# Kernel tuning notes

Hardware: AMD Instinct MI355X
Metric: run time of the kernel (lower is better)

The kernel has to match this reference:

```python
import jax, jax.numpy as jnp
import numpy as np

N = 100000   # nodes
E = 600000   # edges
B = 512      # graphs in batch
H = 128      # hidden dim
ED = 8       # edge feature dim
TWO48 = float(2 ** 48 - 1)


def _w(k, shape, fan_in):
    return jax.random.normal(k, shape, jnp.float32) * (1.0 / np.sqrt(fan_in))


def setup_inputs() -> dict:
    key = jax.random.key(0)
    ks = jax.random.split(key, 32)
    inp = {}
    inp["s_node_ids"] = jax.random.randint(ks[0], (N,), 0, 2 ** 31 - 1, dtype=jnp.int32)
    inp["s_edge_index"] = jax.random.randint(ks[1], (2, E), 0, N, dtype=jnp.int32)
    inp["s_edge_attr"] = jax.random.normal(ks[2], (E, ED), jnp.float32)
    inp["s_batch"] = jnp.sort(jax.random.randint(ks[3], (N,), 0, B, dtype=jnp.int32))
    inp["depth"] = jax.random.uniform(ks[4], (B,), jnp.float32)
    # id_mlp: Linear(1,H) -> ReLU -> Linear(H,H)
    inp["id_w1"] = _w(ks[5], (1, H), 1); inp["id_b1"] = jnp.zeros((H,), jnp.float32)
    inp["id_w2"] = _w(ks[6], (H, H), H); inp["id_b2"] = jnp.zeros((H,), jnp.float32)
    # edge_mlp: Linear(ED,H) -> ReLU -> Linear(H,H)
    inp["ed_w1"] = _w(ks[7], (ED, H), ED); inp["ed_b1"] = jnp.zeros((H,), jnp.float32)
    inp["ed_w2"] = _w(ks[8], (H, H), H); inp["ed_b2"] = jnp.zeros((H,), jnp.float32)
    # GINEConv nn MLPs: Linear(H,H) -> ReLU -> Linear(H,H)
    inp["c1_w1"] = _w(ks[9], (H, H), H); inp["c1_b1"] = jnp.zeros((H,), jnp.float32)
    inp["c1_w2"] = _w(ks[10], (H, H), H); inp["c1_b2"] = jnp.zeros((H,), jnp.float32)
    inp["c2_w1"] = _w(ks[11], (H, H), H); inp["c2_b1"] = jnp.zeros((H,), jnp.float32)
    inp["c2_w2"] = _w(ks[12], (H, H), H); inp["c2_b2"] = jnp.zeros((H,), jnp.float32)
    inp["rg_w1"] = _w(ks[13], (H + 1, H), H + 1); inp["rg_b1"] = jnp.zeros((H,), jnp.float32)
    inp["rg_w2"] = _w(ks[14], (H, 1), H); inp["rg_b2"] = jnp.zeros((1,), jnp.float32)
    return inp


def _mlp2(x, w1, b1, w2, b2):
    return jax.nn.relu(x @ w1 + b1) @ w2 + b2


def _gine(x, src, dst, e, w1, b1, w2, b2):
    # message = ReLU(x_j + e), sum-aggregated at dst; out = nn((1+eps)*x + aggr), eps=0
    msg = jax.nn.relu(x[src] + e)                       # [E, H]
    aggr = jax.ops.segment_sum(msg, dst, num_segments=N)  # [N, H]
    return _mlp2(x + aggr, w1, b1, w2, b2)


def _global_mean(x, batch):
    sums = jax.ops.segment_sum(x, batch, num_segments=B)                          # [B, H]
    cnts = jax.ops.segment_sum(jnp.ones((x.shape[0], 1), x.dtype), batch, num_segments=B)
    return sums / jnp.maximum(cnts, 1.0)


def reference(s_node_ids, s_edge_index, s_edge_attr, s_batch, depth,
              id_w1, id_b1, id_w2, id_b2,
              ed_w1, ed_b1, ed_w2, ed_b2,
              c1_w1, c1_b1, c1_w2, c1_b2,
              c2_w1, c2_b1, c2_w2, c2_b2,
              rg_w1, rg_b1, rg_w2, rg_b2):
    src, dst = s_edge_index[0], s_edge_index[1]
    x0 = jnp.clip(s_node_ids.astype(jnp.float32) / TWO48, 0.0, 1.0)[:, None]  # [N,1]
    x = _mlp2(x0, id_w1, id_b1, id_w2, id_b2)                                 # [N,H]
    e = _mlp2(s_edge_attr, ed_w1, ed_b1, ed_w2, ed_b2)                        # [E,H]
    x = jax.nn.relu(_gine(x, src, dst, e, c1_w1, c1_b1, c1_w2, c1_b2))
    x = jax.nn.relu(_gine(x, src, dst, e, c2_w1, c2_b1, c2_w2, c2_b2))
    rep = jnp.concatenate([_global_mean(x, s_batch), depth[:, None]], axis=1)  # [B,H+1]
    return _mlp2(rep, rg_w1, rg_b1, rg_w2, rg_b2)[:, 0]                        # [B]
```

## Files before the change

kernel.cpp:

```cpp
#include <hip/hip_runtime.h>
#include <hip/hip_bf16.h>

#define N_NODES 100000
#define N_EDGES 600000
#define NB      512
#define H       128
#define ED      8
#define SCAN_CHUNK 1024
#define N_CHUNKS   98

typedef __attribute__((ext_vector_type(8))) short short8;
typedef __attribute__((ext_vector_type(4))) float f32x4;
typedef __attribute__((ext_vector_type(4))) unsigned int u32x4;
typedef unsigned short u16;
typedef unsigned int   u32;

static __device__ __forceinline__ u16 f2bf(float f) {
    u32 u = __float_as_uint(f);
    u32 r = u + 0x7fffu + ((u >> 16) & 1u);
    return (u16)(r >> 16);
}
static __device__ __forceinline__ float bf2f(u32 h) {
    return __uint_as_float(h << 16);
}
static __device__ __forceinline__ u32 bfpack(float lo, float hi) {
    u32 r;
    asm("v_cvt_pk_bf16_f32 %0, %1, %2" : "=v"(r) : "v"(lo), "v"(hi));
    return r;
}

__global__ __launch_bounds__(256) void pack_hist_kernel(
    const float* __restrict__ W0, const float* __restrict__ W1,
    const float* __restrict__ W2, const float* __restrict__ W3,
    const float* __restrict__ W4, const float* __restrict__ W5,
    const float* __restrict__ W6,
    short8* __restrict__ O0, short8* __restrict__ O1,
    short8* __restrict__ O2, short8* __restrict__ O3,
    short8* __restrict__ O4, short8* __restrict__ O5,
    short8* __restrict__ O6,
    const int* __restrict__ edge_index, int* __restrict__ counts)
{
    if (blockIdx.x >= 50) {
        int e = (blockIdx.x - 50) * 256 + threadIdx.x;
        if (e < N_EDGES) atomicAdd(&counts[edge_index[N_EDGES + e]], 1);
        return;
    }
    int gid = blockIdx.x * 256 + threadIdx.x;
    const float* W; short8* O; int Krows, kkmax, slot;
    if (gid < 512) { W = W0; O = O0; Krows = ED; kkmax = 1; slot = gid; }
    else {
        int m = (gid - 512) / 2048;
        slot = (gid - 512) % 2048;
        Krows = H; kkmax = 4;
        switch (m) {
            case 0: W = W1; O = O1; break;
            case 1: W = W2; O = O2; break;
            case 2: W = W3; O = O3; break;
            case 3: W = W4; O = O4; break;
            case 4: W = W5; O = O5; break;
            default: W = W6; O = O6; break;
        }
    }
    int lane = slot & 63;
    int t = slot >> 6;
    int nt = t & 1; t >>= 1;
    int kk = t % kkmax;
    int w  = t / kkmax;
    int quad = lane >> 4, n15 = lane & 15;
    int n = w * 32 + nt * 16 + n15;
    short8 v;
    #pragma unroll
    for (int j = 0; j < 8; j++) {
        int k = kk * 32 + quad * 8 + j;
        v[j] = (k < Krows) ? (short)f2bf(W[k * H + n]) : (short)0;
    }
    O[slot] = v;
}

__global__ __launch_bounds__(256) void scan_node_kernel(
    const int* __restrict__ counts, int* __restrict__ chunk_scan,
    int* __restrict__ bsum_raw,
    const int* __restrict__ ids,
    const float* __restrict__ w1, const float* __restrict__ b1,
    const short8* __restrict__ pW2, const float* __restrict__ b2,
    u16* __restrict__ x_out)
{
    __shared__ u16 sH[64 * 136];
    __shared__ float s_x0[64];
    __shared__ int sS[256];
    int tid = threadIdx.x;

    if (blockIdx.x < N_CHUNKS) {
        int base = blockIdx.x * SCAN_CHUNK + tid * 4;
        int4 v = *(const int4*)&counts[base];
        int q0 = v.x, q1 = q0 + v.y, q2 = q1 + v.z, q3 = q2 + v.w;
        sS[tid] = q3;
        __syncthreads();
        #pragma unroll
        for (int off = 1; off < 256; off <<= 1) {
            int t = (tid >= off) ? sS[tid - off] : 0;
            __syncthreads();
            sS[tid] += t;
            __syncthreads();
        }
        int excl = sS[tid] - q3;
        int4 o;
        o.x = excl; o.y = excl + q0; o.z = excl + q1; o.w = excl + q2;
        *(int4*)&chunk_scan[base] = o;
        if (tid == 255) bsum_raw[blockIdx.x] = sS[255];
        return;
    }

    int bid = blockIdx.x - N_CHUNKS;
    int w = tid >> 6, lane = tid & 63, quad = lane >> 4, n15 = lane & 15;
    short8 fW2[4][2];
    #pragma unroll
    for (int kk = 0; kk < 4; kk++) {
        fW2[kk][0] = pW2[((w * 4 + kk) * 2 + 0) * 64 + lane];
        fW2[kk][1] = pW2[((w * 4 + kk) * 2 + 1) * 64 + lane];
    }
    float rb2[2] = { b2[w * 32 + n15], b2[w * 32 + 16 + n15] };
    float w1c = w1[tid & 127], b1c = b1[tid & 127];
    const int ntile = (N_NODES + 63) / 64;
    for (int tile = bid; tile < ntile; tile += 768) {
        int row0 = tile * 64;
        if (tid < 64) {
            int n = row0 + tid;
            float x0 = (n < N_NODES) ? (float)ids[n] / 281474976710655.0f : 0.0f;
            s_x0[tid] = fminf(fmaxf(x0, 0.0f), 1.0f);
        }
        __syncthreads();
        int half = tid >> 7, c = tid & 127;
        #pragma unroll
        for (int rr = 0; rr < 32; rr += 2) {
            int r = half + rr * 2;
            u32 p = bfpack(fmaxf(s_x0[r] * w1c + b1c, 0.0f),
                           fmaxf(s_x0[r + 2] * w1c + b1c, 0.0f));
            sH[r * 136 + c]       = (u16)p;
            sH[(r + 2) * 136 + c] = (u16)(p >> 16);
        }
        __syncthreads();
        f32x4 acc[4][2];
        #pragma unroll
        for (int s = 0; s < 4; s++) { acc[s][0] = (f32x4){0,0,0,0}; acc[s][1] = (f32x4){0,0,0,0}; }
        #pragma unroll
        for (int kk = 0; kk < 4; kk++) {
            #pragma unroll
            for (int s = 0; s < 4; s++) {
                short8 a = *(const short8*)&sH[(s * 16 + n15) * 136 + kk * 32 + quad * 8];
                acc[s][0] = __builtin_amdgcn_mfma_f32_16x16x32_bf16(a, fW2[kk][0], acc[s][0], 0, 0, 0);
                acc[s][1] = __builtin_amdgcn_mfma_f32_16x16x32_bf16(a, fW2[kk][1], acc[s][1], 0, 0, 0);
            }
        }
        __syncthreads();
        #pragma unroll
        for (int s = 0; s < 4; s++)
            #pragma unroll
            for (int nt = 0; nt < 2; nt++) {
                int col = w * 32 + nt * 16 + n15;
                int rb = (s * 16 + quad * 4) * 136 + col;
                u32 p0 = bfpack(acc[s][nt][0] + rb2[nt], acc[s][nt][1] + rb2[nt]);
                u32 p1 = bfpack(acc[s][nt][2] + rb2[nt], acc[s][nt][3] + rb2[nt]);
                sH[rb]       = (u16)p0;
                sH[rb + 136] = (u16)(p0 >> 16);
                sH[rb + 272] = (u16)p1;
                sH[rb + 408] = (u16)(p1 >> 16);
            }
        __syncthreads();
        for (int idx = tid; idx < 64 * 16; idx += 256) {
            int r = idx >> 4, c8 = (idx & 15) << 3;
            int n = row0 + r;
            if (n < N_NODES)
                *(uint4*)&x_out[(long)n * H + c8] = *(const uint4*)&sH[r * 136 + c8];
        }
        __syncthreads();
    }
}

__global__ __launch_bounds__(256) void fill_kernel(
    const int* __restrict__ edge_index,
    const int* __restrict__ chunk_scan, const int* __restrict__ bsum_raw,
    int* __restrict__ counts, int* __restrict__ src_list,
    const float* __restrict__ attr, u16* __restrict__ attr_perm)
{
    __shared__ int sB[128];
    int tid = threadIdx.x;
    int v0 = 0;
    if (tid < 128) {
        v0 = (tid < N_CHUNKS) ? bsum_raw[tid] : 0;
        sB[tid] = v0;
    }
    __syncthreads();
    #pragma unroll
    for (int off = 1; off < 128; off <<= 1) {
        int t = (tid < 128 && tid >= off) ? sB[tid - off] : 0;
        __syncthreads();
        if (tid < 128) sB[tid] += t;
        __syncthreads();
    }
    if (tid < 128) sB[tid] -= v0;
    __syncthreads();

    int e = blockIdx.x * 256 + tid;
    if (e >= N_EDGES) return;
    int src = edge_index[e];
    int dst = edge_index[N_EDGES + e];
    int slot = atomicAdd(&counts[dst], -1) - 1;
    int pos = chunk_scan[dst] + sB[dst >> 10] + slot;
    src_list[pos] = src;
    float4 a0 = *(const float4*)&attr[(long)e * ED];
    float4 a1 = *(const float4*)&attr[(long)e * ED + 4];
    u32 w0 = bfpack(a0.x, a0.y);
    u32 w1 = bfpack(a0.z, a0.w);
    u32 w2 = bfpack(a1.x, a1.y);
    u32 w3 = bfpack(a1.z, a1.w);
    *(uint4*)&attr_perm[(long)pos * ED] = make_uint4(w0, w1, w2, w3);
}

__global__ __launch_bounds__(256) void edge_mlp_mfma(
    const u16* __restrict__ attr_perm,
    const int* __restrict__ chunk_scan, const int* __restrict__ bsum_raw,
    int* __restrict__ row_start,
    const short8* __restrict__ pW1, const float* __restrict__ b1,
    const short8* __restrict__ pW2, const float* __restrict__ b2,
    u16* __restrict__ e_perm)
{
    __shared__ u16 sH[64 * 136];
    __shared__ int sB[128];
    int tid = threadIdx.x;

    if (blockIdx.x < 392) {
        int v0 = 0;
        if (tid < 128) {
            v0 = (tid < N_CHUNKS) ? bsum_raw[tid] : 0;
            sB[tid] = v0;
        }
        __syncthreads();
        #pragma unroll
        for (int off = 1; off < 128; off <<= 1) {
            int t = (tid < 128 && tid >= off) ? sB[tid - off] : 0;
            __syncthreads();
            if (tid < 128) sB[tid] += t;
            __syncthreads();
        }
        if (tid < 128) sB[tid] -= v0;
        __syncthreads();
        int i = blockIdx.x * 256 + tid;
        if (i <= N_NODES) row_start[i] = chunk_scan[i] + sB[i >> 10];
        __syncthreads();
    }

    int w = tid >> 6, lane = tid & 63, quad = lane >> 4, n15 = lane & 15;
    short8 fW1[2];
    fW1[0] = pW1[(w * 2 + 0) * 64 + lane];
    fW1[1] = pW1[(w * 2 + 1) * 64 + lane];
    short8 fW2[4][2];
    #pragma unroll
    for (int kk = 0; kk < 4; kk++) {
        fW2[kk][0] = pW2[((w * 4 + kk) * 2 + 0) * 64 + lane];
        fW2[kk][1] = pW2[((w * 4 + kk) * 2 + 1) * 64 + lane];
    }
    float rb1[2] = { b1[w * 32 + n15], b1[w * 32 + 16 + n15] };
    float rb2[2] = { b2[w * 32 + n15], b2[w * 32 + 16 + n15] };
    const short8 zero8 = (short8){0,0,0,0,0,0,0,0};
    const int ntile = N_EDGES / 64;
    for (int tile = blockIdx.x; tile < ntile; tile += gridDim.x) {
        int row0 = tile * 64;
        short8 av[4];
        #pragma unroll
        for (int s = 0; s < 4; s++) {
            av[s] = zero8;
            if (quad == 0)
                av[s] = *(const short8*)&attr_perm[(long)(row0 + s * 16 + n15) * ED];
        }
        f32x4 acc[4][2];
        #pragma unroll
        for (int s = 0; s < 4; s++) { acc[s][0] = (f32x4){0,0,0,0}; acc[s][1] = (f32x4){0,0,0,0}; }
        #pragma unroll
        for (int s = 0; s < 4; s++) {
            acc[s][0] = __builtin_amdgcn_mfma_f32_16x16x32_bf16(av[s], fW1[0], acc[s][0], 0, 0, 0);
            acc[s][1] = __builtin_amdgcn_mfma_f32_16x16x32_bf16(av[s], fW1[1], acc[s][1], 0, 0, 0);
        }
        #pragma unroll
        for (int s = 0; s < 4; s++)
            #pragma unroll
            for (int nt = 0; nt < 2; nt++) {
                int col = w * 32 + nt * 16 + n15;
                int rb = (s * 16 + quad * 4) * 136 + col;
                u32 p0 = bfpack(fmaxf(acc[s][nt][0] + rb1[nt], 0.0f),
                                fmaxf(acc[s][nt][1] + rb1[nt], 0.0f));
                u32 p1 = bfpack(fmaxf(acc[s][nt][2] + rb1[nt], 0.0f),
                                fmaxf(acc[s][nt][3] + rb1[nt], 0.0f));
                sH[rb]       = (u16)p0;
                sH[rb + 136] = (u16)(p0 >> 16);
                sH[rb + 272] = (u16)p1;
                sH[rb + 408] = (u16)(p1 >> 16);
            }
        __syncthreads();
        #pragma unroll
        for (int s = 0; s < 4; s++) { acc[s][0] = (f32x4){0,0,0,0}; acc[s][1] = (f32x4){0,0,0,0}; }
        #pragma unroll
        for (int kk = 0; kk < 4; kk++) {
            #pragma unroll
            for (int s = 0; s < 4; s++) {
                short8 a = *(const short8*)&sH[(s * 16 + n15) * 136 + kk * 32 + quad * 8];
                acc[s][0] = __builtin_amdgcn_mfma_f32_16x16x32_bf16(a, fW2[kk][0], acc[s][0], 0, 0, 0);
                acc[s][1] = __builtin_amdgcn_mfma_f32_16x16x32_bf16(a, fW2[kk][1], acc[s][1], 0, 0, 0);
            }
        }
        __syncthreads();
        #pragma unroll
        for (int s = 0; s < 4; s++)
            #pragma unroll
            for (int nt = 0; nt < 2; nt++) {
                int col = w * 32 + nt * 16 + n15;
                int rb = (s * 16 + quad * 4) * 136 + col;
                u32 p0 = bfpack(acc[s][nt][0] + rb2[nt], acc[s][nt][1] + rb2[nt]);
                u32 p1 = bfpack(acc[s][nt][2] + rb2[nt], acc[s][nt][3] + rb2[nt]);
                sH[rb]       = (u16)p0;
                sH[rb + 136] = (u16)(p0 >> 16);
                sH[rb + 272] = (u16)p1;
                sH[rb + 408] = (u16)(p1 >> 16);
            }
        __syncthreads();
        for (int idx = tid; idx < 64 * 16; idx += 256) {
            int r = idx >> 4, c8 = (idx & 15) << 3;
            *(uint4*)&e_perm[(long)(row0 + r) * H + c8] = *(const uint4*)&sH[r * 136 + c8];
        }
        __syncthreads();
    }
}

static __device__ __forceinline__ void acc8(float* a, u32x4 xv, u32x4 ev) {
    #pragma unroll
    for (int q = 0; q < 4; q++) {
        a[2 * q + 0] += fmaxf(bf2f(xv[q] & 0xffff) + bf2f(ev[q] & 0xffff), 0.0f);
        a[2 * q + 1] += fmaxf(bf2f(xv[q] >> 16)    + bf2f(ev[q] >> 16),    0.0f);
    }
}

__global__ __launch_bounds__(256) void aggregate_kernel(
    const int* __restrict__ row_start,
    const int* __restrict__ src_list,
    const u16* __restrict__ e_perm,
    const u16* __restrict__ x,
    u16* __restrict__ xs_out)
{
    int tid  = threadIdx.x;
    int lane = tid & 63;
    int l16  = lane & 15;
    int base = lane & 48;
    int fo   = l16 * 8;
    int n = blockIdx.x * 16 + (tid >> 4);
    const u16* xb = x + fo;

    int beg = row_start[n];
    int end = row_start[n + 1];
    float a[8], b[8];
    #pragma unroll
    for (int q = 0; q < 8; q++) { a[q] = 0.0f; b[q] = 0.0f; }

    for (int j0 = beg; j0 < end; j0 += 16) {
        int m = min(16, end - j0);
        int sv = src_list[j0 + min(l16, m - 1)];
        const u16* ej = e_perm + (long)j0 * H + fo;
        int j = 0;
        for (; j + 2 <= m; j += 2) {
            int s0 = __shfl(sv, base | j);
            int s1 = __shfl(sv, base | (j + 1));
            u32x4 xv0 = *(const u32x4*)(xb + (long)s0 * H);
            u32x4 ev0 = *(const u32x4*)(ej + (long)(j + 0) * H);
            u32x4 xv1 = *(const u32x4*)(xb + (long)s1 * H);
            u32x4 ev1 = *(const u32x4*)(ej + (long)(j + 1) * H);
            acc8(a, xv0, ev0);
            acc8(b, xv1, ev1);
        }
        if (j < m) {
            int s0 = __shfl(sv, base | j);
            u32x4 xv0 = *(const u32x4*)(xb + (long)s0 * H);
            u32x4 ev0 = *(const u32x4*)(ej + (long)j * H);
            acc8(a, xv0, ev0);
        }
    }
    u32x4 xself = *(const u32x4*)(xb + (long)n * H);
    u32x4 out;
    #pragma unroll
    for (int q = 0; q < 4; q++) {
        float o0 = bf2f(xself[q] & 0xffff) + a[2 * q + 0] + b[2 * q + 0];
        float o1 = bf2f(xself[q] >> 16)    + a[2 * q + 1] + b[2 * q + 1];
        out[q] = bfpack(o0, o1);
    }
    *(u32x4*)&xs_out[(long)n * H + fo] = out;
}

__global__ __launch_bounds__(256) void conv_mlp_mfma(
    const u16* __restrict__ xs,
    const short8* __restrict__ pW1, const float* __restrict__ b1,
    const short8* __restrict__ pW2, const float* __restrict__ b2,
    u16* __restrict__ x_out)
{
    __shared__ u16 sA[32 * 136];
    int tid = threadIdx.x;
    int w = tid >> 6, lane = tid & 63, quad = lane >> 4, n15 = lane & 15;
    short8 fW1[4][2], fW2[4][2];
    #pragma unroll
    for (int kk = 0; kk < 4; kk++) {
        fW1[kk][0] = pW1[((w * 4 + kk) * 2 + 0) * 64 + lane];
        fW1[kk][1] = pW1[((w * 4 + kk) * 2 + 1) * 64 + lane];
        fW2[kk][0] = pW2[((w * 4 + kk) * 2 + 0) * 64 + lane];
        fW2[kk][1] = pW2[((w * 4 + kk) * 2 + 1) * 64 + lane];
    }
    float rb1[2] = { b1[w * 32 + n15], b1[w * 32 + 16 + n15] };
    float rb2[2] = { b2[w * 32 + n15], b2[w * 32 + 16 + n15] };
    const int ntile = N_NODES / 32;
    for (int tile = blockIdx.x; tile < ntile; tile += gridDim.x) {
        long row0 = (long)tile * 32;
        for (int idx = tid; idx < 32 * 16; idx += 256) {
            int r = idx >> 4, c8 = (idx & 15) << 3;
            *(uint4*)&sA[r * 136 + c8] = *(const uint4*)&xs[(row0 + r) * H + c8];
        }
        __syncthreads();
        f32x4 acc[2][2];
        #pragma unroll
        for (int s = 0; s < 2; s++) { acc[s][0] = (f32x4){0,0,0,0}; acc[s][1] = (f32x4){0,0,0,0}; }
        #pragma unroll
        for (int kk = 0; kk < 4; kk++) {
            #pragma unroll
            for (int s = 0; s < 2; s++) {
                short8 a = *(const short8*)&sA[(s * 16 + n15) * 136 + kk * 32 + quad * 8];
                acc[s][0] = __builtin_amdgcn_mfma_f32_16x16x32_bf16(a, fW1[kk][0], acc[s][0], 0, 0, 0);
                acc[s][1] = __builtin_amdgcn_mfma_f32_16x16x32_bf16(a, fW1[kk][1], acc[s][1], 0, 0, 0);
            }
        }
        __syncthreads();
        #pragma unroll
        for (int s = 0; s < 2; s++)
            #pragma unroll
            for (int nt = 0; nt < 2; nt++) {
                int col = w * 32 + nt * 16 + n15;
                int rb = (s * 16 + quad * 4) * 136 + col;
                u32 p0 = bfpack(fmaxf(acc[s][nt][0] + rb1[nt], 0.0f),
                                fmaxf(acc[s][nt][1] + rb1[nt], 0.0f));
                u32 p1 = bfpack(fmaxf(acc[s][nt][2] + rb1[nt], 0.0f),
                                fmaxf(acc[s][nt][3] + rb1[nt], 0.0f));
                sA[rb]       = (u16)p0;
                sA[rb + 136] = (u16)(p0 >> 16);
                sA[rb + 272] = (u16)p1;
                sA[rb + 408] = (u16)(p1 >> 16);
            }
        __syncthreads();
        #pragma unroll
        for (int s = 0; s < 2; s++) { acc[s][0] = (f32x4){0,0,0,0}; acc[s][1] = (f32x4){0,0,0,0}; }
        #pragma unroll
        for (int kk = 0; kk < 4; kk++) {
            #pragma unroll
            for (int s = 0; s < 2; s++) {
                short8 a = *(const short8*)&sA[(s * 16 + n15) * 136 + kk * 32 + quad * 8];
                acc[s][0] = __builtin_amdgcn_mfma_f32_16x16x32_bf16(a, fW2[kk][0], acc[s][0], 0, 0, 0);
                acc[s][1] = __builtin_amdgcn_mfma_f32_16x16x32_bf16(a, fW2[kk][1], acc[s][1], 0, 0, 0);
            }
        }
        __syncthreads();
        #pragma unroll
        for (int s = 0; s < 2; s++)
            #pragma unroll
            for (int nt = 0; nt < 2; nt++) {
                int col = w * 32 + nt * 16 + n15;
                int rb = (s * 16 + quad * 4) * 136 + col;
                u32 p0 = bfpack(fmaxf(acc[s][nt][0] + rb2[nt], 0.0f),
                                fmaxf(acc[s][nt][1] + rb2[nt], 0.0f));
                u32 p1 = bfpack(fmaxf(acc[s][nt][2] + rb2[nt], 0.0f),
                                fmaxf(acc[s][nt][3] + rb2[nt], 0.0f));
                sA[rb]       = (u16)p0;
                sA[rb + 136] = (u16)(p0 >> 16);
                sA[rb + 272] = (u16)p1;
                sA[rb + 408] = (u16)(p1 >> 16);
            }
        __syncthreads();
        for (int idx = tid; idx < 32 * 16; idx += 256) {
            int r = idx >> 4, c8 = (idx & 15) << 3;
            *(uint4*)&x_out[(row0 + r) * H + c8] = *(const uint4*)&sA[r * 136 + c8];
        }
        __syncthreads();
    }
}

__global__ __launch_bounds__(256) void pool_kernel(
    const u16* __restrict__ x, const int* __restrict__ batch,
    float* __restrict__ sums, float* __restrict__ cnt)
{
    int sg   = threadIdx.x >> 6;
    int lane = threadIdx.x & 63;
    int fo = lane * 2;
    const int nper = (N_NODES + gridDim.x - 1) / gridDim.x;
    int n0 = blockIdx.x * nper;
    int n1 = min(n0 + nper, N_NODES);
    int cur = -1;
    float a0 = 0.0f, a1 = 0.0f, c = 0.0f;
    for (int n = n0 + sg; n < n1; n += 4) {
        int b = batch[n];
        if (b != cur) {
            if (cur >= 0) {
                atomicAdd(&sums[cur * H + fo],     a0);
                atomicAdd(&sums[cur * H + fo + 1], a1);
                if (lane == 0) atomicAdd(&cnt[cur], c);
            }
            a0 = a1 = 0.0f; c = 0.0f; cur = b;
        }
        u32 xv = *(const u32*)&x[(long)n * H + fo];
        a0 += bf2f(xv & 0xffff);
        a1 += bf2f(xv >> 16);
        c += 1.0f;
    }
    if (cur >= 0) {
        atomicAdd(&sums[cur * H + fo],     a0);
        atomicAdd(&sums[cur * H + fo + 1], a1);
        if (lane == 0) atomicAdd(&cnt[cur], c);
    }
}

__global__ __launch_bounds__(128) void regressor_kernel(
    const float* __restrict__ sums, const float* __restrict__ cnt,
    const float* __restrict__ depth,
    const float* __restrict__ w1, const float* __restrict__ b1,
    const float* __restrict__ w2, const float* __restrict__ b2,
    float* __restrict__ out)
{
    __shared__ float s_mean[H];
    __shared__ float s_red[2];
    int b = blockIdx.x;
    int j = threadIdx.x;
    float c = fmaxf(cnt[b], 1.0f);
    s_mean[j] = sums[b * H + j] / c;
    __syncthreads();
    float h = b1[j];
    #pragma unroll 8
    for (int k = 0; k < H; k++) h += s_mean[k] * w1[k * H + j];
    h += depth[b] * w1[H * H + j];
    h = fmaxf(h, 0.0f);
    float p = h * w2[j];
    #pragma unroll
    for (int off = 32; off >= 1; off >>= 1) p += __shfl_down(p, off, 64);
    if ((j & 63) == 0) s_red[j >> 6] = p;
    __syncthreads();
    if (j == 0) out[b] = s_red[0] + s_red[1] + b2[0];
}

extern "C" void kernel_launch(void* const* d_in, const int* in_sizes, int n_in,
                              void* d_out, int out_size, void* d_ws, size_t ws_size,
                              hipStream_t stream)
{
    const int*   ids   = (const int*)  d_in[0];
    const int*   eidx  = (const int*)  d_in[1];
    const float* eattr = (const float*)d_in[2];
    const int*   batch = (const int*)  d_in[3];
    const float* depth = (const float*)d_in[4];
    const float* id_w1 = (const float*)d_in[5];
    const float* id_b1 = (const float*)d_in[6];
    const float* id_w2 = (const float*)d_in[7];
    const float* id_b2 = (const float*)d_in[8];
    const float* ed_w1 = (const float*)d_in[9];
    const float* ed_b1 = (const float*)d_in[10];
    const float* ed_w2 = (const float*)d_in[11];
    const float* ed_b2 = (const float*)d_in[12];
    const float* c1_w1 = (const float*)d_in[13];
    const float* c1_b1 = (const float*)d_in[14];
    const float* c1_w2 = (const float*)d_in[15];
    const float* c1_b2 = (const float*)d_in[16];
    const float* c2_w1 = (const float*)d_in[17];
    const float* c2_b1 = (const float*)d_in[18];
    const float* c2_w2 = (const float*)d_in[19];
    const float* c2_b2 = (const float*)d_in[20];
    const float* rg_w1 = (const float*)d_in[21];
    const float* rg_b1 = (const float*)d_in[22];
    const float* rg_w2 = (const float*)d_in[23];
    const float* rg_b2 = (const float*)d_in[24];

    char* ws = (char*)d_ws;
    u16*   e_buf    = (u16*)  (ws);
    u16*   x_buf    = (u16*)  (ws + 153600000);
    u16*   xs_buf   = (u16*)  (ws + 179200000);
    float* sums_buf = (float*)(ws + 204800000);
    float* cnt_buf  = (float*)(ws + 205062144);
    int*   counts   = (int*)  (ws + 205064192);
    int*   chunk_sc = (int*)  (ws + 205465600);
    int*   bsum_raw = (int*)  (ws + 205867008);
    int*   src_list = (int*)  (ws + 205868032);
    short8* ed_w1p  = (short8*)(ws + 208268032);
    short8* ed_w2p  = (short8*)(ws + 208276224);
    short8* c1_w1p  = (short8*)(ws + 208308992);
    short8* c1_w2p  = (short8*)(ws + 208341760);
    short8* c2_w1p  = (short8*)(ws + 208374528);
    short8* c2_w2p  = (short8*)(ws + 208407296);
    short8* id_w2p  = (short8*)(ws + 208440064);
    int*   row_start = counts;
    u16*   attr_perm = xs_buf;

    hipMemsetAsync(counts, 0, 401408, stream);
    hipMemsetAsync(sums_buf, 0, (size_t)(NB * H + NB) * 4, stream);

    pack_hist_kernel<<<50 + (N_EDGES + 255) / 256, 256, 0, stream>>>(
        ed_w1, ed_w2, c1_w1, c1_w2, c2_w1, c2_w2, id_w2,
        ed_w1p, ed_w2p, c1_w1p, c1_w2p, c2_w1p, c2_w2p, id_w2p,
        eidx, counts);

    scan_node_kernel<<<N_CHUNKS + 768, 256, 0, stream>>>(
        counts, chunk_sc, bsum_raw,
        ids, id_w1, id_b1, id_w2p, id_b2, x_buf);

    fill_kernel<<<(N_EDGES + 255) / 256, 256, 0, stream>>>(
        eidx, chunk_sc, bsum_raw, counts, src_list, eattr, attr_perm);

    edge_mlp_mfma<<<2048, 256, 0, stream>>>(
        attr_perm, chunk_sc, bsum_raw, row_start,
        ed_w1p, ed_b1, ed_w2p, ed_b2, e_buf);

    aggregate_kernel<<<6250, 256, 0, stream>>>(row_start, src_list, e_buf, x_buf, xs_buf);
    conv_mlp_mfma<<<3125, 256, 0, stream>>>(xs_buf, c1_w1p, c1_b1, c1_w2p, c1_b2, x_buf);

    aggregate_kernel<<<6250, 256, 0, stream>>>(row_start, src_list, e_buf, x_buf, xs_buf);
    conv_mlp_mfma<<<3125, 256, 0, stream>>>(xs_buf, c2_w1p, c2_b1, c2_w2p, c2_b2, x_buf);

    pool_kernel<<<2048, 256, 0, stream>>>(x_buf, batch, sums_buf, cnt_buf);
    regressor_kernel<<<NB, 128, 0, stream>>>(sums_buf, cnt_buf, depth,
                                             rg_w1, rg_b1, rg_w2, rg_b2, (float*)d_out);
}
```

Before: 393.3 us.

## Fuse GINE neighbor aggregation with the two-layer conv MLP per 16-node tile

Merges the aggregate kernel and the MFMA conv MLP into one kernel. Each block aggregates 16 nodes into shared memory and then runs both 128x128 bf16 MFMA layers on that tile before writing the result. This removes the xs intermediate write and read through global memory and drops two launches. In exchange, weights are reloaded from global or cache by every one of 6250 blocks, the MFMA tile shrinks to 16 rows, and the matmul waits on the slowest neighbor list in the block.

```diff
diff --git a/kernel.cpp b/kernel.cpp
--- a/kernel.cpp
+++ b/kernel.cpp
@@ -339,19 +339,23 @@
     }
 }
 
-__global__ __launch_bounds__(256) void aggregate_kernel(
+__global__ __launch_bounds__(256) void gine_fused(
     const int* __restrict__ row_start,
     const int* __restrict__ src_list,
     const u16* __restrict__ e_perm,
     const u16* __restrict__ x,
-    u16* __restrict__ xs_out)
-{
+    const short8* __restrict__ pW1, const float* __restrict__ b1,
+    const short8* __restrict__ pW2, const float* __restrict__ b2,
+    u16* __restrict__ x_out)
+{
+    __shared__ u16 sA[16 * 136];
     int tid  = threadIdx.x;
     int lane = tid & 63;
     int l16  = lane & 15;
     int base = lane & 48;
     int fo   = l16 * 8;
-    int n = blockIdx.x * 16 + (tid >> 4);
+    int r    = tid >> 4;
+    int n    = blockIdx.x * 16 + r;
     const u16* xb = x + fo;
 
     int beg = row_start[n];
@@ -383,105 +387,72 @@
         }
     }
     u32x4 xself = *(const u32x4*)(xb + (long)n * H);
-    u32x4 out;
+    u32x4 xsrow;
     #pragma unroll
     for (int q = 0; q < 4; q++) {
         float o0 = bf2f(xself[q] & 0xffff) + a[2 * q + 0] + b[2 * q + 0];
         float o1 = bf2f(xself[q] >> 16)    + a[2 * q + 1] + b[2 * q + 1];
-        out[q] = bfpack(o0, o1);
-    }
-    *(u32x4*)&xs_out[(long)n * H + fo] = out;
-}
-
-__global__ __launch_bounds__(256) void conv_mlp_mfma(
-    const u16* __restrict__ xs,
-    const short8* __restrict__ pW1, const float* __restrict__ b1,
-    const short8* __restrict__ pW2, const float* __restrict__ b2,
-    u16* __restrict__ x_out)
-{
-    __shared__ u16 sA[32 * 136];
-    int tid = threadIdx.x;
-    int w = tid >> 6, lane = tid & 63, quad = lane >> 4, n15 = lane & 15;
-    short8 fW1[4][2], fW2[4][2];
-    #pragma unroll
-    for (int kk = 0; kk < 4; kk++) {
-        fW1[kk][0] = pW1[((w * 4 + kk) * 2 + 0) * 64 + lane];
-        fW1[kk][1] = pW1[((w * 4 + kk) * 2 + 1) * 64 + lane];
-        fW2[kk][0] = pW2[((w * 4 + kk) * 2 + 0) * 64 + lane];
-        fW2[kk][1] = pW2[((w * 4 + kk) * 2 + 1) * 64 + lane];
-    }
+        xsrow[q] = bfpack(o0, o1);
+    }
+    *(uint4*)&sA[r * 136 + fo] = *(uint4*)&xsrow;
+    __syncthreads();
+
+    int w = tid >> 6, quad = lane >> 4, n15 = l16;
     float rb1[2] = { b1[w * 32 + n15], b1[w * 32 + 16 + n15] };
     float rb2[2] = { b2[w * 32 + n15], b2[w * 32 + 16 + n15] };
-    const int ntile = N_NODES / 32;
-    for (int tile = blockIdx.x; tile < ntile; tile += gridDim.x) {
-        long row0 = (long)tile * 32;
-        for (int idx = tid; idx < 32 * 16; idx += 256) {
-            int r = idx >> 4, c8 = (idx & 15) << 3;
-            *(uint4*)&sA[r * 136 + c8] = *(const uint4*)&xs[(row0 + r) * H + c8];
-        }
-        __syncthreads();
-        f32x4 acc[2][2];
-        #pragma unroll
-        for (int s = 0; s < 2; s++) { acc[s][0] = (f32x4){0,0,0,0}; acc[s][1] = (f32x4){0,0,0,0}; }
-        #pragma unroll
-        for (int kk = 0; kk < 4; kk++) {
-            #pragma unroll
-            for (int s = 0; s < 2; s++) {
-                short8 a = *(const short8*)&sA[(s * 16 + n15) * 136 + kk * 32 + quad * 8];
-                acc[s][0] = __builtin_amdgcn_mfma_f32_16x16x32_bf16(a, fW1[kk][0], acc[s][0], 0, 0, 0);
-                acc[s][1] = __builtin_amdgcn_mfma_f32_16x16x32_bf16(a, fW1[kk][1], acc[s][1], 0, 0, 0);
-            }
-        }
-        __syncthreads();
-        #pragma unroll
-        for (int s = 0; s < 2; s++)
-            #pragma unroll
-            for (int nt = 0; nt < 2; nt++) {
-                int col = w * 32 + nt * 16 + n15;
-                int rb = (s * 16 + quad * 4) * 136 + col;
-                u32 p0 = bfpack(fmaxf(acc[s][nt][0] + rb1[nt], 0.0f),
-                                fmaxf(acc[s][nt][1] + rb1[nt], 0.0f));
-                u32 p1 = bfpack(fmaxf(acc[s][nt][2] + rb1[nt], 0.0f),
-                                fmaxf(acc[s][nt][3] + rb1[nt], 0.0f));
-                sA[rb]       = (u16)p0;
-                sA[rb + 136] = (u16)(p0 >> 16);
-                sA[rb + 272] = (u16)p1;
-                sA[rb + 408] = (u16)(p1 >> 16);
-            }
-        __syncthreads();
-        #pragma unroll
-        for (int s = 0; s < 2; s++) { acc[s][0] = (f32x4){0,0,0,0}; acc[s][1] = (f32x4){0,0,0,0}; }
-        #pragma unroll
-        for (int kk = 0; kk < 4; kk++) {
-            #pragma unroll
-            for (int s = 0; s < 2; s++) {
-                short8 a = *(const short8*)&sA[(s * 16 + n15) * 136 + kk * 32 + quad * 8];
-                acc[s][0] = __builtin_amdgcn_mfma_f32_16x16x32_bf16(a, fW2[kk][0], acc[s][0], 0, 0, 0);
-                acc[s][1] = __builtin_amdgcn_mfma_f32_16x16x32_bf16(a, fW2[kk][1], acc[s][1], 0, 0, 0);
-            }
-        }
-        __syncthreads();
-        #pragma unroll
-        for (int s = 0; s < 2; s++)
-            #pragma unroll
-            for (int nt = 0; nt < 2; nt++) {
-                int col = w * 32 + nt * 16 + n15;
-                int rb = (s * 16 + quad * 4) * 136 + col;
-                u32 p0 = bfpack(fmaxf(acc[s][nt][0] + rb2[nt], 0.0f),
-                                fmaxf(acc[s][nt][1] + rb2[nt], 0.0f));
-                u32 p1 = bfpack(fmaxf(acc[s][nt][2] + rb2[nt], 0.0f),
-                                fmaxf(acc[s][nt][3] + rb2[nt], 0.0f));
-                sA[rb]       = (u16)p0;
-                sA[rb + 136] = (u16)(p0 >> 16);
-                sA[rb + 272] = (u16)p1;
-                sA[rb + 408] = (u16)(p1 >> 16);
-            }
-        __syncthreads();
-        for (int idx = tid; idx < 32 * 16; idx += 256) {
-            int r = idx >> 4, c8 = (idx & 15) << 3;
-            *(uint4*)&x_out[(row0 + r) * H + c8] = *(const uint4*)&sA[r * 136 + c8];
-        }
-        __syncthreads();
+    f32x4 acc[2];
+    acc[0] = (f32x4){0,0,0,0}; acc[1] = (f32x4){0,0,0,0};
+    #pragma unroll
+    for (int kk = 0; kk < 4; kk++) {
+        short8 av = *(const short8*)&sA[n15 * 136 + kk * 32 + quad * 8];
+        short8 w0 = pW1[((w * 4 + kk) * 2 + 0) * 64 + lane];
+        short8 w1v = pW1[((w * 4 + kk) * 2 + 1) * 64 + lane];
+        acc[0] = __builtin_amdgcn_mfma_f32_16x16x32_bf16(av, w0, acc[0], 0, 0, 0);
+        acc[1] = __builtin_amdgcn_mfma_f32_16x16x32_bf16(av, w1v, acc[1], 0, 0, 0);
+    }
+    __syncthreads();
+    #pragma unroll
+    for (int nt = 0; nt < 2; nt++) {
+        int col = w * 32 + nt * 16 + n15;
+        int rb = (quad * 4) * 136 + col;
+        u32 p0 = bfpack(fmaxf(acc[nt][0] + rb1[nt], 0.0f),
+                        fmaxf(acc[nt][1] + rb1[nt], 0.0f));
+        u32 p1 = bfpack(fmaxf(acc[nt][2] + rb1[nt], 0.0f),
+                        fmaxf(acc[nt][3] + rb1[nt], 0.0f));
+        sA[rb]       = (u16)p0;
+        sA[rb + 136] = (u16)(p0 >> 16);
+        sA[rb + 272] = (u16)p1;
+        sA[rb + 408] = (u16)(p1 >> 16);
+    }
+    __syncthreads();
+    acc[0] = (f32x4){0,0,0,0}; acc[1] = (f32x4){0,0,0,0};
+    #pragma unroll
+    for (int kk = 0; kk < 4; kk++) {
+        short8 av = *(const short8*)&sA[n15 * 136 + kk * 32 + quad * 8];
+        short8 w0 = pW2[((w * 4 + kk) * 2 + 0) * 64 + lane];
+        short8 w1v = pW2[((w * 4 + kk) * 2 + 1) * 64 + lane];
+        acc[0] = __builtin_amdgcn_mfma_f32_16x16x32_bf16(av, w0, acc[0], 0, 0, 0);
+        acc[1] = __builtin_amdgcn_mfma_f32_16x16x32_bf16(av, w1v, acc[1], 0, 0, 0);
+    }
+    __syncthreads();
+    #pragma unroll
+    for (int nt = 0; nt < 2; nt++) {
+        int col = w * 32 + nt * 16 + n15;
+        int rb = (quad * 4) * 136 + col;
+        u32 p0 = bfpack(fmaxf(acc[nt][0] + rb2[nt], 0.0f),
+                        fmaxf(acc[nt][1] + rb2[nt], 0.0f));
+        u32 p1 = bfpack(fmaxf(acc[nt][2] + rb2[nt], 0.0f),
+                        fmaxf(acc[nt][3] + rb2[nt], 0.0f));
+        sA[rb]       = (u16)p0;
+        sA[rb + 136] = (u16)(p0 >> 16);
+        sA[rb + 272] = (u16)p1;
+        sA[rb + 408] = (u16)(p1 >> 16);
+    }
+    __syncthreads();
+    {
+        int rr = tid >> 4, c8 = (tid & 15) << 3;
+        int nn = blockIdx.x * 16 + rr;
+        *(uint4*)&x_out[(long)nn * H + c8] = *(const uint4*)&sA[rr * 136 + c8];
     }
 }
 
@@ -615,11 +586,10 @@
         attr_perm, chunk_sc, bsum_raw, row_start,
         ed_w1p, ed_b1, ed_w2p, ed_b2, e_buf);
 
-    aggregate_kernel<<<6250, 256, 0, stream>>>(row_start, src_list, e_buf, x_buf, xs_buf);
-    conv_mlp_mfma<<<3125, 256, 0, stream>>>(xs_buf, c1_w1p, c1_b1, c1_w2p, c1_b2, x_buf);
-
-    aggregate_kernel<<<6250, 256, 0, stream>>>(row_start, src_list, e_buf, x_buf, xs_buf);
-    conv_mlp_mfma<<<3125, 256, 0, stream>>>(xs_buf, c2_w1p, c2_b1, c2_w2p, c2_b2, x_buf);
+    gine_fused<<<6250, 256, 0, stream>>>(row_start, src_list, e_buf, x_buf,
+                                         c1_w1p, c1_b1, c1_w2p, c1_b2, xs_buf);
+    gine_fused<<<6250, 256, 0, stream>>>(row_start, src_list, e_buf, xs_buf,
+                                         c2_w1p, c2_b1, c2_w2p, c2_b2, x_buf);
 
     pool_kernel<<<2048, 256, 0, stream>>>(x_buf, batch, sums_buf, cnt_buf);
     regressor_kernel<<<NB, 128, 0, stream>>>(sums_buf, cnt_buf, depth,
```

New measurement: 370.3 us. 1.06x faster.
